# Kernel optimization log

Hardware: AMD Instinct MI355X
Metric: run time of the kernel (lower is better)

## Reference

```python
import math
import jax, jax.numpy as jnp
import numpy as np

S = 2048
HIDDEN = 5120
H = 16              # num_local_heads (128 global heads / TP=8)
NOPE, ROPE, V = 128, 64, 128
QK = NOPE + ROPE    # 192 (module pads to 256; zero-pad is a mathematical no-op)
QLORA, KVLORA = 1536, 512
EPS = 1e-6
BASE, FACTOR = 10000.0, 40.0
BETA_FAST, BETA_SLOW = 32.0, 1.0
ORIG_MAX = 4096
MSCALE = MSCALE_ALL = 0.707


def _yarn_get_mscale(scale, mscale):
    if scale <= 1:
        return 1.0
    return 0.1 * mscale * math.log(scale) + 1.0


SCALING = QK ** -0.5 * _yarn_get_mscale(FACTOR, MSCALE_ALL) ** 2
COS_SIN_MSCALE = _yarn_get_mscale(FACTOR, MSCALE) / _yarn_get_mscale(FACTOR, MSCALE_ALL)


def _yarn_inv_freq():
    half = ROPE // 2
    i = np.arange(half, dtype=np.float64)
    pos_freqs = BASE ** (2.0 * i / ROPE)
    inv_extra = 1.0 / pos_freqs
    inv_interp = 1.0 / (FACTOR * pos_freqs)

    def corr_dim(n_rot):
        return ROPE * math.log(ORIG_MAX / (n_rot * 2 * math.pi)) / (2 * math.log(BASE))

    low = max(math.floor(corr_dim(BETA_FAST)), 0)
    high = min(math.ceil(corr_dim(BETA_SLOW)), ROPE - 1)
    ramp = np.clip((i - low) / max(high - low, 1e-3), 0.0, 1.0)
    inv_freq_mask = 1.0 - ramp  # 1 -> extrapolation, 0 -> interpolation
    inv_freq = inv_interp * (1.0 - inv_freq_mask) + inv_extra * inv_freq_mask
    return jnp.asarray(inv_freq, dtype=jnp.float32)


INV_FREQ = _yarn_inv_freq()  # [ROPE/2]


def _apply_rope(x, cos, sin):
    # non-neox (interleaved pairs): x [S, heads, ROPE], cos/sin [S, ROPE/2]
    x1 = x[..., 0::2]
    x2 = x[..., 1::2]
    c = cos[:, None, :]
    s = sin[:, None, :]
    o1 = x1 * c - x2 * s
    o2 = x2 * c + x1 * s
    return jnp.stack([o1, o2], axis=-1).reshape(x.shape)


def _rms_norm(x, w):
    var = jnp.mean(x.astype(jnp.float32) ** 2, axis=-1, keepdims=True)
    return (x.astype(jnp.float32) * jax.lax.rsqrt(var + EPS)).astype(x.dtype) * w


def setup_inputs() -> dict:
    key = jax.random.key(0)
    ks = jax.random.split(key, 8)
    sd = 0.02
    return {
        'positions': jnp.arange(S, dtype=jnp.int64 if jax.config.jax_enable_x64 else jnp.int32),
        'hidden_states': jax.random.normal(ks[0], (S, HIDDEN), jnp.float32),
        'w_q_a': jax.random.normal(ks[1], (HIDDEN, QLORA), jnp.float32) * sd,
        'q_a_ln_w': jnp.ones((QLORA,), jnp.float32),
        'w_q_b': jax.random.normal(ks[2], (QLORA, H * QK), jnp.float32) * sd,
        'w_kv_a': jax.random.normal(ks[3], (HIDDEN, KVLORA + ROPE), jnp.float32) * sd,
        'kv_a_ln_w': jnp.ones((KVLORA,), jnp.float32),
        'w_kv_b': jax.random.normal(ks[4], (KVLORA, H * (NOPE + V)), jnp.float32) * sd,
        'w_o': jax.random.normal(ks[5], (H * V, HIDDEN), jnp.float32) * sd,
    }


def reference(positions, hidden_states, w_q_a, q_a_ln_w, w_q_b, w_kv_a, kv_a_ln_w, w_kv_b, w_o):
    # Q low-rank path: q_a_proj -> RMSNorm -> q_b_proj
    q = hidden_states @ w_q_a                       # [S, QLORA]
    q = _rms_norm(q, q_a_ln_w)
    q = (q @ w_q_b).reshape(S, H, QK)               # [S, H, 192]
    q_nope, q_pe = q[..., :NOPE], q[..., NOPE:]

    # KV latent path: shared MQA latent + decoupled rope key
    latent = hidden_states @ w_kv_a                 # [S, KVLORA+ROPE]
    kv_a = _rms_norm(latent[:, :KVLORA], kv_a_ln_w)
    k_pe = latent[:, None, KVLORA:]                 # [S, 1, ROPE]
    kv = (kv_a @ w_kv_b).reshape(S, H, NOPE + V)
    k_nope, v = kv[..., :NOPE], kv[..., NOPE:]

    # partial (decoupled) yarn RoPE on the 64-dim rope slice
    freqs = positions.astype(jnp.float32)[:, None] * INV_FREQ[None, :]
    cos = jnp.cos(freqs) * COS_SIN_MSCALE
    sin = jnp.sin(freqs) * COS_SIN_MSCALE
    q_pe = _apply_rope(q_pe, cos, sin)
    k_pe = _apply_rope(k_pe, cos, sin)

    qf = jnp.concatenate([q_nope, q_pe], axis=-1)   # [S, H, 192]
    kf = jnp.concatenate([k_nope, jnp.broadcast_to(k_pe, (S, H, ROPE))], axis=-1)

    # causal paged-attention prefill; zero-padding head dims to 256 is a no-op
    scores = jnp.einsum('qhd,khd->hqk', qf, kf) * SCALING  # [H, S, S]
    causal = jnp.tril(jnp.ones((S, S), dtype=bool))
    scores = jnp.where(causal[None], scores, -jnp.inf)
    probs = jax.nn.softmax(scores, axis=-1)
    attn = jnp.einsum('hqk,khd->qhd', probs, v).reshape(S, H * V)
    return attn @ w_o                               # [S, HIDDEN]
```

## Files before the change

### kernel.cpp

```cpp
#include <hip/hip_runtime.h>
#include <math.h>

typedef unsigned short u16;
typedef unsigned int u32;
typedef __attribute__((ext_vector_type(4))) float f32x4;
typedef __attribute__((ext_vector_type(8))) unsigned short u16x8;
typedef __attribute__((ext_vector_type(4))) unsigned short u16x4;
typedef __attribute__((ext_vector_type(8))) __bf16 bf16x8;

#define DEV __device__ __forceinline__

constexpr int S = 2048;
constexpr int HIDDEN = 5120;
constexpr int H = 16;
constexpr int NOPE = 128, ROPE_D = 64, VD = 128;
constexpr int QKD = NOPE + ROPE_D;
constexpr int QLORA = 1536, KVLORA = 512;
constexpr int KVA_N = KVLORA + ROPE_D;
constexpr float SCALING = 0.11472134f;

DEV u16 f2b(float f) {
  u32 u = __builtin_bit_cast(u32, f);
  u32 r = u + 0x7FFFu + ((u >> 16) & 1u);
  return (u16)(r >> 16);
}
DEV float b2f(u16 h) { return __builtin_bit_cast(float, (u32)h << 16); }

DEV void store_out(float* p, float v) { *p = v; }
DEV void store_out(u16* p, float v) { *p = f2b(v); }

DEV void gload_lds16(const u16* g, u16* l) {
  auto* gp = (const __attribute__((address_space(1))) u16*)g;
  auto* lp = (__attribute__((address_space(3))) u16*)l;
  __builtin_amdgcn_global_load_lds(gp, lp, 16, 0, 0);
}

#define SWZ(row, col) ((col) ^ (((row) & 7) << 3))

__global__ __launch_bounds__(256) void k_convert(const float* __restrict__ in,
                                                 u16* __restrict__ out, int n) {
  int i = (blockIdx.x * 256 + threadIdx.x) * 4;
  if (i >= n) return;
  f32x4 v = *reinterpret_cast<const f32x4*>(in + i);
  u16x4 o;
  o[0] = f2b(v[0]); o[1] = f2b(v[1]); o[2] = f2b(v[2]); o[3] = f2b(v[3]);
  *reinterpret_cast<u16x4*>(out + i) = o;
}

__global__ __launch_bounds__(256) void k_transpose(const float* __restrict__ in,
                                                   u16* __restrict__ out, int R, int C) {
  __shared__ float t[32][33];
  int c0 = blockIdx.x * 32, r0 = blockIdx.y * 32;
  int tx = threadIdx.x, ty = threadIdx.y;
  for (int r = ty; r < 32; r += 8)
    t[r][tx] = in[(size_t)(r0 + r) * C + c0 + tx];
  __syncthreads();
  for (int r = ty; r < 32; r += 8)
    out[(size_t)(c0 + r) * R + r0 + tx] = f2b(t[tx][r]);
}

__global__ __launch_bounds__(256) void k_rope_tables(float* __restrict__ cs,
                                                     float* __restrict__ sn) {
  int idx = blockIdx.x * 256 + threadIdx.x;
  if (idx >= S * 32) return;
  int s = idx >> 5, j = idx & 31;
  double pf = pow(10000.0, (double)j / 32.0);
  double inv_extra = 1.0 / pf;
  double inv_interp = 1.0 / (40.0 * pf);
  double twopi = 6.283185307179586476925286766559;
  double lnb2 = 2.0 * log(10000.0);
  double lowd = floor(64.0 * log(4096.0 / (32.0 * twopi)) / lnb2);
  if (lowd < 0.0) lowd = 0.0;
  double highd = ceil(64.0 * log(4096.0 / twopi) / lnb2);
  if (highd > 63.0) highd = 63.0;
  double denom = highd - lowd;
  if (denom < 0.001) denom = 0.001;
  double ramp = ((double)j - lowd) / denom;
  ramp = ramp < 0.0 ? 0.0 : (ramp > 1.0 ? 1.0 : ramp);
  float invf = (float)(inv_interp * ramp + inv_extra * (1.0 - ramp));
  float fr = (float)s * invf;
  cs[idx] = cosf(fr);
  sn[idx] = sinf(fr);
}

template <typename OutT>
DEV void gemm_body(u16* Al, u16* Bl, const u16* __restrict__ A,
                   const u16* __restrict__ BT, OutT* __restrict__ C,
                   int N, int K, int mbase, int nbase) {
  const int tid = threadIdx.x;
  const int lane = tid & 63, wave = tid >> 6;
  const int wr = wave >> 1, wc = wave & 1;
  const int lr = lane & 15, lk = lane >> 4;
  const int srow = wave * 32 + (lane >> 2);
  const int skoff = (lane & 3) * 8;
  const u16* aptr = A + (size_t)(mbase + srow) * K + skoff;
  const u16* bptr = BT + (size_t)(nbase + srow) * K + skoff;
  u16* alw = Al + wave * (32 * 32);
  u16* blw = Bl + wave * (32 * 32);

  auto STAGE = [&](int b, int kk) {
    gload_lds16(aptr + kk, alw + b * 4096);
    gload_lds16(aptr + (size_t)16 * K + kk, alw + b * 4096 + 16 * 32);
    gload_lds16(bptr + kk, blw + b * 4096);
    gload_lds16(bptr + (size_t)16 * K + kk, blw + b * 4096 + 16 * 32);
  };

  f32x4 acc[4][4];
#pragma unroll
  for (int mf = 0; mf < 4; ++mf)
#pragma unroll
    for (int nf = 0; nf < 4; ++nf) acc[mf][nf] = {0.f, 0.f, 0.f, 0.f};

  const int nt = K >> 5;
  STAGE(0, 0);
  STAGE(1, 32);
  for (int t = 0; t < nt; ++t) {
    const int cur = t & 1;
    if (t + 1 < nt)
      asm volatile("s_waitcnt vmcnt(4)" ::: "memory");
    else
      asm volatile("s_waitcnt vmcnt(0)" ::: "memory");
    __builtin_amdgcn_s_barrier();
    const u16* Ac = Al + cur * 4096;
    const u16* Bc = Bl + cur * 4096;
    bf16x8 af[4], bfr[4];
#pragma unroll
    for (int mf = 0; mf < 4; ++mf)
      af[mf] = *reinterpret_cast<const bf16x8*>(Ac + (wr * 64 + mf * 16 + lr) * 32 + lk * 8);
#pragma unroll
    for (int nf = 0; nf < 4; ++nf)
      bfr[nf] = *reinterpret_cast<const bf16x8*>(Bc + (wc * 64 + nf * 16 + lr) * 32 + lk * 8);
#pragma unroll
    for (int mf = 0; mf < 4; ++mf)
#pragma unroll
      for (int nf = 0; nf < 4; ++nf)
        acc[mf][nf] = __builtin_amdgcn_mfma_f32_16x16x32_bf16(af[mf], bfr[nf], acc[mf][nf], 0, 0, 0);
    __builtin_amdgcn_s_barrier();
    if (t + 2 < nt) STAGE(cur, (t + 2) * 32);
  }

#pragma unroll
  for (int mf = 0; mf < 4; ++mf)
#pragma unroll
    for (int nf = 0; nf < 4; ++nf) {
      int col = nbase + wc * 64 + nf * 16 + lr;
      if (col < N) {
#pragma unroll
        for (int r = 0; r < 4; ++r) {
          int row = mbase + wr * 64 + mf * 16 + lk * 4 + r;
          store_out(&C[(size_t)row * N + col], acc[mf][nf][r]);
        }
      }
    }
}

template <typename OutT>
__global__ __launch_bounds__(256) void k_gemm(const u16* __restrict__ A,
                                              const u16* __restrict__ BT,
                                              OutT* __restrict__ C, int N, int K) {
  __shared__ u16 Al[2 * 128 * 32];
  __shared__ u16 Bl[2 * 128 * 32];
  gemm_body(Al, Bl, A, BT, C, N, K, blockIdx.y * 128, blockIdx.x * 128);
}

template <typename OutT>
__global__ __launch_bounds__(256) void k_gemm2(const u16* __restrict__ A0, const u16* __restrict__ B0,
                                               OutT* __restrict__ C0, int N0, int K0, int nbx0,
                                               const u16* __restrict__ A1, const u16* __restrict__ B1,
                                               OutT* __restrict__ C1, int N1, int K1) {
  __shared__ u16 Al[2 * 128 * 32];
  __shared__ u16 Bl[2 * 128 * 32];
  int bx = blockIdx.x;
  if (bx < nbx0)
    gemm_body(Al, Bl, A0, B0, C0, N0, K0, blockIdx.y * 128, bx * 128);
  else
    gemm_body(Al, Bl, A1, B1, C1, N1, K1, blockIdx.y * 128, (bx - nbx0) * 128);
}

__global__ __launch_bounds__(256) void k_rmsnorm(const float* __restrict__ x,
                                                 const float* __restrict__ w,
                                                 u16* __restrict__ y, int ncols, int instride) {
  int row = blockIdx.x, tid = threadIdx.x;
  const float* xr = x + (size_t)row * instride;
  float ss = 0.f;
  for (int i = tid * 4; i < ncols; i += 1024) {
    f32x4 v = *reinterpret_cast<const f32x4*>(xr + i);
    ss += v[0] * v[0] + v[1] * v[1] + v[2] * v[2] + v[3] * v[3];
  }
  for (int off = 32; off > 0; off >>= 1) ss += __shfl_down(ss, off);
  __shared__ float red[4];
  if ((tid & 63) == 0) red[tid >> 6] = ss;
  __syncthreads();
  ss = red[0] + red[1] + red[2] + red[3];
  float sc = rsqrtf(ss / (float)ncols + 1e-6f);
  u16* yr = y + (size_t)row * ncols;
  for (int i = tid * 4; i < ncols; i += 1024) {
    f32x4 v = *reinterpret_cast<const f32x4*>(xr + i);
    u16x4 o;
    o[0] = f2b(v[0] * sc * w[i]);
    o[1] = f2b(v[1] * sc * w[i + 1]);
    o[2] = f2b(v[2] * sc * w[i + 2]);
    o[3] = f2b(v[3] * sc * w[i + 3]);
    *reinterpret_cast<u16x4*>(yr + i) = o;
  }
}

__global__ __launch_bounds__(256) void k_build_qkf(const u16* __restrict__ qn,
                                                   const u16* __restrict__ kv,
                                                   const float* __restrict__ latent,
                                                   const float* __restrict__ cs,
                                                   const float* __restrict__ sn,
                                                   u16* __restrict__ qf, u16* __restrict__ kf) {
  int s = blockIdx.x, tid = threadIdx.x;
  for (int idx = tid; idx < H * NOPE; idx += 256) {
    int h = idx >> 7, dd = idx & 127;
    qf[((size_t)h * S + s) * QKD + dd] = qn[(size_t)s * (H * QKD) + h * QKD + dd];
    kf[((size_t)h * S + s) * QKD + dd] = kv[(size_t)s * (H * 256) + h * 256 + dd];
  }
  for (int idx = tid; idx < H * 32; idx += 256) {
    int h = idx >> 5, j = idx & 31;
    float c = cs[s * 32 + j], si = sn[s * 32 + j];
    float x1 = b2f(qn[(size_t)s * (H * QKD) + h * QKD + NOPE + 2 * j]);
    float x2 = b2f(qn[(size_t)s * (H * QKD) + h * QKD + NOPE + 2 * j + 1]);
    qf[((size_t)h * S + s) * QKD + NOPE + 2 * j] = f2b(x1 * c - x2 * si);
    qf[((size_t)h * S + s) * QKD + NOPE + 2 * j + 1] = f2b(x2 * c + x1 * si);
    float k1 = latent[(size_t)s * KVA_N + KVLORA + 2 * j];
    float k2 = latent[(size_t)s * KVA_N + KVLORA + 2 * j + 1];
    kf[((size_t)h * S + s) * QKD + NOPE + 2 * j] = f2b(k1 * c - k2 * si);
    kf[((size_t)h * S + s) * QKD + NOPE + 2 * j + 1] = f2b(k2 * c + k1 * si);
  }
}

__global__ void k_build_vt(const u16* __restrict__ kv, u16* __restrict__ vt) {
  __shared__ u16 t[32][33];
  int s0 = blockIdx.x * 32, d0 = blockIdx.y * 32, h = blockIdx.z;
  int tx = threadIdx.x, ty = threadIdx.y;
  for (int r = ty; r < 32; r += 8)
    t[r][tx] = kv[(size_t)(s0 + r) * (H * 256) + h * 256 + NOPE + d0 + tx];
  __syncthreads();
  for (int r = ty; r < 32; r += 8)
    vt[((size_t)h * VD + d0 + r) * S + s0 + tx] = t[tx][r];
}

__global__ __launch_bounds__(256) void k_attn(const u16* __restrict__ qf,
                                              const u16* __restrict__ kf,
                                              const u16* __restrict__ vt,
                                              u16* __restrict__ attn) {
  const int bidx = blockIdx.x;
  const int j = bidx & 31;
  const int h = bidx >> 5;
  const int qt = (h < 8) ? j : 31 - j;
  const int qbase = qt * 64;
  const int tid = threadIdx.x, wave = tid >> 6, lane = tid & 63;
  const int lr = lane & 15, lk = lane >> 4;
  __shared__ u16 Kl[64][192];
  __shared__ u16 Vl[128][64];
  __shared__ u16 Pl[4][16][64];

  int krow_[6], kofs_[6], vrow_[4], vofs_[4];
#pragma unroll
  for (int i = 0; i < 6; ++i) { int c = tid + i * 256; krow_[i] = c / 24; kofs_[i] = (c % 24) * 8; }
#pragma unroll
  for (int i = 0; i < 4; ++i) { int c = tid + i * 256; vrow_[i] = c >> 3; vofs_[i] = (c & 7) * 8; }
  const u16* kfh = kf + (size_t)h * S * QKD;
  const u16* vth = vt + (size_t)h * VD * S;

  bf16x8 qfrag[6];
  const u16* qrow = qf + ((size_t)h * S + qbase + wave * 16 + lr) * QKD;
#pragma unroll
  for (int d = 0; d < 6; ++d)
    qfrag[d] = *reinterpret_cast<const bf16x8*>(qrow + d * 32 + lk * 8);

  u16x8 kreg[6], vreg[4];
#pragma unroll
  for (int i = 0; i < 6; ++i)
    kreg[i] = *reinterpret_cast<const u16x8*>(kfh + (size_t)krow_[i] * QKD + kofs_[i]);
#pragma unroll
  for (int i = 0; i < 4; ++i)
    vreg[i] = *reinterpret_cast<const u16x8*>(vth + (size_t)vrow_[i] * S + vofs_[i]);

  f32x4 o[8];
#pragma unroll
  for (int f = 0; f < 8; ++f) o[f] = {0.f, 0.f, 0.f, 0.f};
  float m_[4] = {-__builtin_inff(), -__builtin_inff(), -__builtin_inff(), -__builtin_inff()};
  float l_[4] = {0.f, 0.f, 0.f, 0.f};

  const int ktiles = qt + 1;
  for (int kt = 0; kt < ktiles; ++kt) {
    const int kbase = kt * 64;
    __builtin_amdgcn_s_barrier();
#pragma unroll
    for (int i = 0; i < 6; ++i)
      *reinterpret_cast<u16x8*>(&Kl[krow_[i]][SWZ(krow_[i], kofs_[i])]) = kreg[i];
#pragma unroll
    for (int i = 0; i < 4; ++i)
      *reinterpret_cast<u16x8*>(&Vl[vrow_[i]][SWZ(vrow_[i], vofs_[i])]) = vreg[i];
    if (kt + 1 < ktiles) {
      const int nb = kbase + 64;
#pragma unroll
      for (int i = 0; i < 6; ++i)
        kreg[i] = *reinterpret_cast<const u16x8*>(kfh + (size_t)(nb + krow_[i]) * QKD + kofs_[i]);
#pragma unroll
      for (int i = 0; i < 4; ++i)
        vreg[i] = *reinterpret_cast<const u16x8*>(vth + (size_t)vrow_[i] * S + nb + vofs_[i]);
    }
    asm volatile("s_waitcnt lgkmcnt(0)" ::: "memory");
    __builtin_amdgcn_s_barrier();

    f32x4 sacc[4];
#pragma unroll
    for (int nf = 0; nf < 4; ++nf) sacc[nf] = {0.f, 0.f, 0.f, 0.f};
    __builtin_amdgcn_s_setprio(1);
#pragma unroll
    for (int nf = 0; nf < 4; ++nf)
#pragma unroll
      for (int dk = 0; dk < 6; ++dk) {
        int krow = nf * 16 + lr;
        bf16x8 b = *reinterpret_cast<const bf16x8*>(&Kl[krow][SWZ(krow, dk * 32 + lk * 8)]);
        sacc[nf] = __builtin_amdgcn_mfma_f32_16x16x32_bf16(qfrag[dk], b, sacc[nf], 0, 0, 0);
      }
    __builtin_amdgcn_s_setprio(0);

    float sv[4][4];
    float rowmax[4] = {-__builtin_inff(), -__builtin_inff(), -__builtin_inff(), -__builtin_inff()};
#pragma unroll
    for (int nf = 0; nf < 4; ++nf) {
      int kcol = kbase + nf * 16 + lr;
#pragma unroll
      for (int r = 0; r < 4; ++r) {
        float v = sacc[nf][r] * SCALING;
        int qrow_g = qbase + wave * 16 + lk * 4 + r;
        if (kcol > qrow_g) v = -__builtin_inff();
        sv[nf][r] = v;
        rowmax[r] = fmaxf(rowmax[r], v);
      }
    }
#pragma unroll
    for (int r = 0; r < 4; ++r) {
#pragma unroll
      for (int off = 1; off < 16; off <<= 1)
        rowmax[r] = fmaxf(rowmax[r], __shfl_xor(rowmax[r], off));
    }
    float alpha[4], rowsum[4] = {0.f, 0.f, 0.f, 0.f};
#pragma unroll
    for (int r = 0; r < 4; ++r) {
      float mn = fmaxf(m_[r], rowmax[r]);
      alpha[r] = __expf(m_[r] - mn);
      m_[r] = mn;
    }
#pragma unroll
    for (int nf = 0; nf < 4; ++nf)
#pragma unroll
      for (int r = 0; r < 4; ++r) {
        float p = __expf(sv[nf][r] - m_[r]);
        sv[nf][r] = p;
        rowsum[r] += p;
      }
#pragma unroll
    for (int r = 0; r < 4; ++r) {
#pragma unroll
      for (int off = 1; off < 16; off <<= 1) rowsum[r] += __shfl_xor(rowsum[r], off);
      l_[r] = l_[r] * alpha[r] + rowsum[r];
    }
#pragma unroll
    for (int nf = 0; nf < 4; ++nf)
#pragma unroll
      for (int r = 0; r < 4; ++r) {
        int prow = lk * 4 + r;
        Pl[wave][prow][SWZ(prow, nf * 16 + lr)] = f2b(sv[nf][r]);
      }
#pragma unroll
    for (int f = 0; f < 8; ++f)
#pragma unroll
      for (int r = 0; r < 4; ++r) o[f][r] *= alpha[r];

    __builtin_amdgcn_s_setprio(1);
#pragma unroll
    for (int kk = 0; kk < 2; ++kk) {
      bf16x8 pa = *reinterpret_cast<const bf16x8*>(&Pl[wave][lr][SWZ(lr, kk * 32 + lk * 8)]);
#pragma unroll
      for (int f = 0; f < 8; ++f) {
        int vrow = f * 16 + lr;
        bf16x8 b = *reinterpret_cast<const bf16x8*>(&Vl[vrow][SWZ(vrow, kk * 32 + lk * 8)]);
        o[f] = __builtin_amdgcn_mfma_f32_16x16x32_bf16(pa, b, o[f], 0, 0, 0);
      }
    }
    __builtin_amdgcn_s_setprio(0);
  }

#pragma unroll
  for (int f = 0; f < 8; ++f)
#pragma unroll
    for (int r = 0; r < 4; ++r) {
      int row = qbase + wave * 16 + lk * 4 + r;
      float val = o[f][r] / l_[r];
      attn[(size_t)row * (H * VD) + h * VD + f * 16 + lr] = f2b(val);
    }
}

extern "C" void kernel_launch(void* const* d_in, const int* in_sizes, int n_in,
                              void* d_out, int out_size, void* d_ws, size_t ws_size,
                              hipStream_t stream) {
  (void)in_sizes; (void)n_in; (void)out_size; (void)ws_size;
  const float* hidden    = (const float*)d_in[1];
  const float* w_q_a     = (const float*)d_in[2];
  const float* q_a_ln_w  = (const float*)d_in[3];
  const float* w_q_b     = (const float*)d_in[4];
  const float* w_kv_a    = (const float*)d_in[5];
  const float* kv_a_ln_w = (const float*)d_in[6];
  const float* w_kv_b    = (const float*)d_in[7];
  const float* w_o       = (const float*)d_in[8];
  float* out = (float*)d_out;

  char* ws = (char*)d_ws;
  size_t off = 0;
  auto alloc = [&](size_t bytes) {
    size_t o = off;
    off += (bytes + 255) & ~(size_t)255;
    return o;
  };
  constexpr int KVA_PAD = 640;
  size_t o_hs    = alloc((size_t)S * HIDDEN * 2);
  size_t o_btqa  = alloc((size_t)QLORA * HIDDEN * 2);
  size_t o_btkva = alloc((size_t)KVA_PAD * HIDDEN * 2);
  size_t o_btqb  = alloc((size_t)(H * QKD) * QLORA * 2);
  size_t o_btkvb = alloc((size_t)(H * 256) * KVLORA * 2);
  size_t o_qlat  = alloc((size_t)S * QLORA * 4);
  size_t o_lat   = alloc((size_t)S * KVA_N * 4);
  size_t o_qln   = alloc((size_t)S * QLORA * 2);
  size_t o_kvln  = alloc((size_t)S * KVLORA * 2);
  size_t o_qn    = alloc((size_t)S * (H * QKD) * 2);
  size_t o_kv    = alloc((size_t)S * (H * 256) * 2);
  size_t o_kf    = alloc((size_t)H * S * QKD * 2);
  size_t o_vt    = alloc((size_t)H * VD * S * 2);
  size_t o_cs    = alloc((size_t)S * 32 * 4);
  size_t o_sn    = alloc((size_t)S * 32 * 4);

  u16* hs_bf  = (u16*)(ws + o_hs);
  u16* bt_qa  = (u16*)(ws + o_btqa);
  u16* bt_kva = (u16*)(ws + o_btkva);
  u16* bt_qb  = (u16*)(ws + o_btqb);
  u16* bt_kvb = (u16*)(ws + o_btkvb);
  float* q_lat  = (float*)(ws + o_qlat);
  float* latent = (float*)(ws + o_lat);
  u16* q_ln  = (u16*)(ws + o_qln);
  u16* kv_ln = (u16*)(ws + o_kvln);
  u16* qn    = (u16*)(ws + o_qn);
  u16* kvb   = (u16*)(ws + o_kv);
  u16* kf    = (u16*)(ws + o_kf);
  u16* vt    = (u16*)(ws + o_vt);
  float* cs = (float*)(ws + o_cs);
  float* sn = (float*)(ws + o_sn);
  u16* qf   = (u16*)(ws + o_hs);
  u16* bt_o = (u16*)(ws + o_btqa);
  u16* attn = (u16*)(ws + o_qlat);

  dim3 t256(256), t32x8(32, 8);

  k_convert<<<(S * HIDDEN / 4 + 255) / 256, t256, 0, stream>>>(hidden, hs_bf, S * HIDDEN);
  k_transpose<<<dim3(QLORA / 32, HIDDEN / 32), t32x8, 0, stream>>>(w_q_a, bt_qa, HIDDEN, QLORA);
  k_transpose<<<dim3(KVA_N / 32, HIDDEN / 32), t32x8, 0, stream>>>(w_kv_a, bt_kva, HIDDEN, KVA_N);
  k_transpose<<<dim3(H * QKD / 32, QLORA / 32), t32x8, 0, stream>>>(w_q_b, bt_qb, QLORA, H * QKD);
  k_transpose<<<dim3(H * 256 / 32, KVLORA / 32), t32x8, 0, stream>>>(w_kv_b, bt_kvb, KVLORA, H * 256);
  k_rope_tables<<<(S * 32 + 255) / 256, t256, 0, stream>>>(cs, sn);

  k_gemm2<float><<<dim3(QLORA / 128 + KVA_PAD / 128, S / 128), t256, 0, stream>>>(
      hs_bf, bt_qa, q_lat, QLORA, HIDDEN, QLORA / 128,
      hs_bf, bt_kva, latent, KVA_N, HIDDEN);

  k_rmsnorm<<<S, t256, 0, stream>>>(q_lat, q_a_ln_w, q_ln, QLORA, QLORA);
  k_rmsnorm<<<S, t256, 0, stream>>>(latent, kv_a_ln_w, kv_ln, KVLORA, KVA_N);

  k_gemm2<u16><<<dim3((H * QKD) / 128 + (H * 256) / 128, S / 128), t256, 0, stream>>>(
      q_ln, bt_qb, qn, H * QKD, QLORA, (H * QKD) / 128,
      kv_ln, bt_kvb, kvb, H * 256, KVLORA);

  k_build_qkf<<<S, t256, 0, stream>>>(qn, kvb, latent, cs, sn, qf, kf);
  k_build_vt<<<dim3(S / 32, VD / 32, H), t32x8, 0, stream>>>(kvb, vt);

  k_transpose<<<dim3(HIDDEN / 32, (H * VD) / 32), t32x8, 0, stream>>>(w_o, bt_o, H * VD, HIDDEN);

  k_attn<<<dim3(512), t256, 0, stream>>>(qf, kf, vt, attn);

  k_gemm<float><<<dim3(HIDDEN / 128, S / 128), t256, 0, stream>>>(attn, bt_o, out, S * 0 + HIDDEN, H * VD);
}
```

Measured before the change: 380.6 us.

## Split-K the first projection GEMM and swizzle GEMM LDS layout

The first down-projection GEMM is split into two K halves, writing separate fp32 partial outputs that are summed inside the RMSNorm and RoPE-building kernels. This doubles the block count so the grid fills the CUs better. Separately, the LDS tile layout of all GEMMs gets an XOR swizzle on the k-chunk index to reduce bank conflicts on fragment reads. The cost is extra partial-buffer memory traffic and workspace.

```diff
diff --git a/kernel.cpp b/kernel.cpp
--- a/kernel.cpp
+++ b/kernel.cpp
@@ -86,23 +86,24 @@
 template <typename OutT>
 DEV void gemm_body(u16* Al, u16* Bl, const u16* __restrict__ A,
                    const u16* __restrict__ BT, OutT* __restrict__ C,
-                   int N, int K, int mbase, int nbase) {
+                   int N, int Kstride, int Klen, int mbase, int nbase) {
   const int tid = threadIdx.x;
   const int lane = tid & 63, wave = tid >> 6;
   const int wr = wave >> 1, wc = wave & 1;
   const int lr = lane & 15, lk = lane >> 4;
   const int srow = wave * 32 + (lane >> 2);
-  const int skoff = (lane & 3) * 8;
-  const u16* aptr = A + (size_t)(mbase + srow) * K + skoff;
-  const u16* bptr = BT + (size_t)(nbase + srow) * K + skoff;
+  const int skoff = (((lane & 3) ^ ((lane >> 3) & 3))) * 8;
+  const int swlk8 = (lk ^ ((lr >> 1) & 3)) * 8;
+  const u16* aptr = A + (size_t)(mbase + srow) * Kstride + skoff;
+  const u16* bptr = BT + (size_t)(nbase + srow) * Kstride + skoff;
   u16* alw = Al + wave * (32 * 32);
   u16* blw = Bl + wave * (32 * 32);
 
   auto STAGE = [&](int b, int kk) {
     gload_lds16(aptr + kk, alw + b * 4096);
-    gload_lds16(aptr + (size_t)16 * K + kk, alw + b * 4096 + 16 * 32);
+    gload_lds16(aptr + (size_t)16 * Kstride + kk, alw + b * 4096 + 16 * 32);
     gload_lds16(bptr + kk, blw + b * 4096);
-    gload_lds16(bptr + (size_t)16 * K + kk, blw + b * 4096 + 16 * 32);
+    gload_lds16(bptr + (size_t)16 * Kstride + kk, blw + b * 4096 + 16 * 32);
   };
 
   f32x4 acc[4][4];
@@ -111,7 +112,7 @@
 #pragma unroll
     for (int nf = 0; nf < 4; ++nf) acc[mf][nf] = {0.f, 0.f, 0.f, 0.f};
 
-  const int nt = K >> 5;
+  const int nt = Klen >> 5;
   STAGE(0, 0);
   STAGE(1, 32);
   for (int t = 0; t < nt; ++t) {
@@ -126,10 +127,10 @@
     bf16x8 af[4], bfr[4];
 #pragma unroll
     for (int mf = 0; mf < 4; ++mf)
-      af[mf] = *reinterpret_cast<const bf16x8*>(Ac + (wr * 64 + mf * 16 + lr) * 32 + lk * 8);
+      af[mf] = *reinterpret_cast<const bf16x8*>(Ac + (wr * 64 + mf * 16 + lr) * 32 + swlk8);
 #pragma unroll
     for (int nf = 0; nf < 4; ++nf)
-      bfr[nf] = *reinterpret_cast<const bf16x8*>(Bc + (wc * 64 + nf * 16 + lr) * 32 + lk * 8);
+      bfr[nf] = *reinterpret_cast<const bf16x8*>(Bc + (wc * 64 + nf * 16 + lr) * 32 + swlk8);
 #pragma unroll
     for (int mf = 0; mf < 4; ++mf)
 #pragma unroll
@@ -160,7 +161,7 @@
                                               OutT* __restrict__ C, int N, int K) {
   __shared__ u16 Al[2 * 128 * 32];
   __shared__ u16 Bl[2 * 128 * 32];
-  gemm_body(Al, Bl, A, BT, C, N, K, blockIdx.y * 128, blockIdx.x * 128);
+  gemm_body(Al, Bl, A, BT, C, N, K, K, blockIdx.y * 128, blockIdx.x * 128);
 }
 
 template <typename OutT>
@@ -172,19 +173,44 @@
   __shared__ u16 Bl[2 * 128 * 32];
   int bx = blockIdx.x;
   if (bx < nbx0)
-    gemm_body(Al, Bl, A0, B0, C0, N0, K0, blockIdx.y * 128, bx * 128);
+    gemm_body(Al, Bl, A0, B0, C0, N0, K0, K0, blockIdx.y * 128, bx * 128);
   else
-    gemm_body(Al, Bl, A1, B1, C1, N1, K1, blockIdx.y * 128, (bx - nbx0) * 128);
-}
-
-__global__ __launch_bounds__(256) void k_rmsnorm(const float* __restrict__ x,
-                                                 const float* __restrict__ w,
-                                                 u16* __restrict__ y, int ncols, int instride) {
+    gemm_body(Al, Bl, A1, B1, C1, N1, K1, K1, blockIdx.y * 128, (bx - nbx0) * 128);
+}
+
+__global__ __launch_bounds__(256) void k_gemm_dp(const u16* __restrict__ A,
+                                                 const u16* __restrict__ Bq,
+                                                 const u16* __restrict__ Bkv,
+                                                 float* __restrict__ q0, float* __restrict__ q1,
+                                                 float* __restrict__ l0, float* __restrict__ l1) {
+  __shared__ u16 Al[2 * 128 * 32];
+  __shared__ u16 Bl[2 * 128 * 32];
+  constexpr int KH = HIDDEN / 2;
+  int bx = blockIdx.x;
+  int split = bx >= 17;
+  int j = bx - split * 17;
+  const u16* As = A + split * KH;
+  if (j < 12) {
+    gemm_body(Al, Bl, As, Bq + split * KH, split ? q1 : q0, QLORA, HIDDEN, KH,
+              blockIdx.y * 128, j * 128);
+  } else {
+    gemm_body(Al, Bl, As, Bkv + split * KH, split ? l1 : l0, KVA_N, HIDDEN, KH,
+              blockIdx.y * 128, (j - 12) * 128);
+  }
+}
+
+__global__ __launch_bounds__(256) void k_rmsnorm2(const float* __restrict__ x0,
+                                                  const float* __restrict__ x1,
+                                                  const float* __restrict__ w,
+                                                  u16* __restrict__ y, int ncols, int instride) {
   int row = blockIdx.x, tid = threadIdx.x;
-  const float* xr = x + (size_t)row * instride;
+  const float* xr0 = x0 + (size_t)row * instride;
+  const float* xr1 = x1 + (size_t)row * instride;
   float ss = 0.f;
   for (int i = tid * 4; i < ncols; i += 1024) {
-    f32x4 v = *reinterpret_cast<const f32x4*>(xr + i);
+    f32x4 a = *reinterpret_cast<const f32x4*>(xr0 + i);
+    f32x4 b = *reinterpret_cast<const f32x4*>(xr1 + i);
+    f32x4 v = a + b;
     ss += v[0] * v[0] + v[1] * v[1] + v[2] * v[2] + v[3] * v[3];
   }
   for (int off = 32; off > 0; off >>= 1) ss += __shfl_down(ss, off);
@@ -195,7 +221,9 @@
   float sc = rsqrtf(ss / (float)ncols + 1e-6f);
   u16* yr = y + (size_t)row * ncols;
   for (int i = tid * 4; i < ncols; i += 1024) {
-    f32x4 v = *reinterpret_cast<const f32x4*>(xr + i);
+    f32x4 a = *reinterpret_cast<const f32x4*>(xr0 + i);
+    f32x4 b = *reinterpret_cast<const f32x4*>(xr1 + i);
+    f32x4 v = a + b;
     u16x4 o;
     o[0] = f2b(v[0] * sc * w[i]);
     o[1] = f2b(v[1] * sc * w[i + 1]);
@@ -207,7 +235,8 @@
 
 __global__ __launch_bounds__(256) void k_build_qkf(const u16* __restrict__ qn,
                                                    const u16* __restrict__ kv,
-                                                   const float* __restrict__ latent,
+                                                   const float* __restrict__ lat0,
+                                                   const float* __restrict__ lat1,
                                                    const float* __restrict__ cs,
                                                    const float* __restrict__ sn,
                                                    u16* __restrict__ qf, u16* __restrict__ kf) {
@@ -224,8 +253,8 @@
     float x2 = b2f(qn[(size_t)s * (H * QKD) + h * QKD + NOPE + 2 * j + 1]);
     qf[((size_t)h * S + s) * QKD + NOPE + 2 * j] = f2b(x1 * c - x2 * si);
     qf[((size_t)h * S + s) * QKD + NOPE + 2 * j + 1] = f2b(x2 * c + x1 * si);
-    float k1 = latent[(size_t)s * KVA_N + KVLORA + 2 * j];
-    float k2 = latent[(size_t)s * KVA_N + KVLORA + 2 * j + 1];
+    float k1 = lat0[(size_t)s * KVA_N + KVLORA + 2 * j] + lat1[(size_t)s * KVA_N + KVLORA + 2 * j];
+    float k2 = lat0[(size_t)s * KVA_N + KVLORA + 2 * j + 1] + lat1[(size_t)s * KVA_N + KVLORA + 2 * j + 1];
     kf[((size_t)h * S + s) * QKD + NOPE + 2 * j] = f2b(k1 * c - k2 * si);
     kf[((size_t)h * S + s) * QKD + NOPE + 2 * j + 1] = f2b(k2 * c + k1 * si);
   }
@@ -425,8 +454,10 @@
   size_t o_btkva = alloc((size_t)KVA_PAD * HIDDEN * 2);
   size_t o_btqb  = alloc((size_t)(H * QKD) * QLORA * 2);
   size_t o_btkvb = alloc((size_t)(H * 256) * KVLORA * 2);
-  size_t o_qlat  = alloc((size_t)S * QLORA * 4);
-  size_t o_lat   = alloc((size_t)S * KVA_N * 4);
+  size_t o_qlat0 = alloc((size_t)S * QLORA * 4);
+  size_t o_qlat1 = alloc((size_t)S * QLORA * 4);
+  size_t o_lat0  = alloc((size_t)S * KVA_N * 4);
+  size_t o_lat1  = alloc((size_t)S * KVA_N * 4);
   size_t o_qln   = alloc((size_t)S * QLORA * 2);
   size_t o_kvln  = alloc((size_t)S * KVLORA * 2);
   size_t o_qn    = alloc((size_t)S * (H * QKD) * 2);
@@ -441,8 +472,10 @@
   u16* bt_kva = (u16*)(ws + o_btkva);
   u16* bt_qb  = (u16*)(ws + o_btqb);
   u16* bt_kvb = (u16*)(ws + o_btkvb);
-  float* q_lat  = (float*)(ws + o_qlat);
-  float* latent = (float*)(ws + o_lat);
+  float* q_lat0 = (float*)(ws + o_qlat0);
+  float* q_lat1 = (float*)(ws + o_qlat1);
+  float* lat0   = (float*)(ws + o_lat0);
+  float* lat1   = (float*)(ws + o_lat1);
   u16* q_ln  = (u16*)(ws + o_qln);
   u16* kv_ln = (u16*)(ws + o_kvln);
   u16* qn    = (u16*)(ws + o_qn);
@@ -453,7 +486,7 @@
   float* sn = (float*)(ws + o_sn);
   u16* qf   = (u16*)(ws + o_hs);
   u16* bt_o = (u16*)(ws + o_btqa);
-  u16* attn = (u16*)(ws + o_qlat);
+  u16* attn = (u16*)(ws + o_qlat0);
 
   dim3 t256(256), t32x8(32, 8);
 
@@ -464,23 +497,22 @@
   k_transpose<<<dim3(H * 256 / 32, KVLORA / 32), t32x8, 0, stream>>>(w_kv_b, bt_kvb, KVLORA, H * 256);
   k_rope_tables<<<(S * 32 + 255) / 256, t256, 0, stream>>>(cs, sn);
 
-  k_gemm2<float><<<dim3(QLORA / 128 + KVA_PAD / 128, S / 128), t256, 0, stream>>>(
-      hs_bf, bt_qa, q_lat, QLORA, HIDDEN, QLORA / 128,
-      hs_bf, bt_kva, latent, KVA_N, HIDDEN);
-
-  k_rmsnorm<<<S, t256, 0, stream>>>(q_lat, q_a_ln_w, q_ln, QLORA, QLORA);
-  k_rmsnorm<<<S, t256, 0, stream>>>(latent, kv_a_ln_w, kv_ln, KVLORA, KVA_N);
+  k_gemm_dp<<<dim3(34, S / 128), t256, 0, stream>>>(hs_bf, bt_qa, bt_kva,
+                                                    q_lat0, q_lat1, lat0, lat1);
+
+  k_rmsnorm2<<<S, t256, 0, stream>>>(q_lat0, q_lat1, q_a_ln_w, q_ln, QLORA, QLORA);
+  k_rmsnorm2<<<S, t256, 0, stream>>>(lat0, lat1, kv_a_ln_w, kv_ln, KVLORA, KVA_N);
 
   k_gemm2<u16><<<dim3((H * QKD) / 128 + (H * 256) / 128, S / 128), t256, 0, stream>>>(
       q_ln, bt_qb, qn, H * QKD, QLORA, (H * QKD) / 128,
       kv_ln, bt_kvb, kvb, H * 256, KVLORA);
 
-  k_build_qkf<<<S, t256, 0, stream>>>(qn, kvb, latent, cs, sn, qf, kf);
+  k_build_qkf<<<S, t256, 0, stream>>>(qn, kvb, lat0, lat1, cs, sn, qf, kf);
   k_build_vt<<<dim3(S / 32, VD / 32, H), t32x8, 0, stream>>>(kvb, vt);
 
   k_transpose<<<dim3(HIDDEN / 32, (H * VD) / 32), t32x8, 0, stream>>>(w_o, bt_o, H * VD, HIDDEN);
 
   k_attn<<<dim3(512), t256, 0, stream>>>(qf, kf, vt, attn);
 
-  k_gemm<float><<<dim3(HIDDEN / 128, S / 128), t256, 0, stream>>>(attn, bt_o, out, S * 0 + HIDDEN, H * VD);
-}
+  k_gemm<float><<<dim3(HIDDEN / 128, S / 128), t256, 0, stream>>>(attn, bt_o, out, HIDDEN, H * VD);
+}
```

New measurement: 378.3 us. No clear change (-0.6%).

## Enlarge GEMM tiles to 256-wide with 4-stage pipeline, LDS swizzle, 8 waves

Applied to the files above, without the earlier changes.

Rewrites the shared GEMM body to use 512-thread blocks with 128x256 or 256x256 tiles and a 4-deep global-to-LDS prefetch ring. It also XOR-swizzles the LDS layout to avoid bank conflicts and raises wave priority around the MFMA loop. The projection GEMMs get dedicated kernels with flattened grids sized to the new tiles, and the kv_a weight padding grows to 768 to fit 256-wide column tiles. The aim is more data reuse per tile and better latency hiding, at the cost of more LDS per block and fewer blocks, which may leave CUs idle on the smaller GEMMs.

```diff
diff --git a/kernel.cpp b/kernel.cpp
--- a/kernel.cpp
+++ b/kernel.cpp
@@ -83,98 +83,133 @@
   sn[idx] = sinf(fr);
 }
 
-template <typename OutT>
+template <int BM, typename OutT>
 DEV void gemm_body(u16* Al, u16* Bl, const u16* __restrict__ A,
                    const u16* __restrict__ BT, OutT* __restrict__ C,
                    int N, int K, int mbase, int nbase) {
+  constexpr int MF = BM / 32;
+  constexpr int ABUF = BM * 32;
+  constexpr int BBUF = 256 * 32;
+  constexpr int L = (BM == 256) ? 4 : 3;
   const int tid = threadIdx.x;
   const int lane = tid & 63, wave = tid >> 6;
-  const int wr = wave >> 1, wc = wave & 1;
+  const int wm = wave >> 2, wn = wave & 3;
   const int lr = lane & 15, lk = lane >> 4;
-  const int srow = wave * 32 + (lane >> 2);
-  const int skoff = (lane & 3) * 8;
-  const u16* aptr = A + (size_t)(mbase + srow) * K + skoff;
-  const u16* bptr = BT + (size_t)(nbase + srow) * K + skoff;
-  u16* alw = Al + wave * (32 * 32);
-  u16* blw = Bl + wave * (32 * 32);
+  const int srowB = wave * 32 + (lane >> 2);
+  const int srowA = (BM == 256) ? srowB : (wave * 16 + (lane >> 2));
+  const int skoff = ((lane & 3) ^ ((lane >> 3) & 3)) * 8;
+  const int swlk8 = (lk ^ ((lr >> 1) & 3)) * 8;
+  const u16* aptr = A + (size_t)(mbase + srowA) * K + skoff;
+  const u16* bptr = BT + (size_t)(nbase + srowB) * K + skoff;
+  u16* alw = Al + wave * ((BM == 256) ? 1024 : 512);
+  u16* blw = Bl + wave * 1024;
 
   auto STAGE = [&](int b, int kk) {
-    gload_lds16(aptr + kk, alw + b * 4096);
-    gload_lds16(aptr + (size_t)16 * K + kk, alw + b * 4096 + 16 * 32);
-    gload_lds16(bptr + kk, blw + b * 4096);
-    gload_lds16(bptr + (size_t)16 * K + kk, blw + b * 4096 + 16 * 32);
+    gload_lds16(aptr + kk, alw + b * ABUF);
+    if constexpr (BM == 256) gload_lds16(aptr + (size_t)16 * K + kk, alw + b * ABUF + 512);
+    gload_lds16(bptr + kk, blw + b * BBUF);
+    gload_lds16(bptr + (size_t)16 * K + kk, blw + b * BBUF + 512);
   };
 
-  f32x4 acc[4][4];
-#pragma unroll
-  for (int mf = 0; mf < 4; ++mf)
+  f32x4 acc[MF][4];
+#pragma unroll
+  for (int mf = 0; mf < MF; ++mf)
 #pragma unroll
     for (int nf = 0; nf < 4; ++nf) acc[mf][nf] = {0.f, 0.f, 0.f, 0.f};
 
   const int nt = K >> 5;
   STAGE(0, 0);
   STAGE(1, 32);
+  STAGE(2, 64);
+  STAGE(3, 96);
   for (int t = 0; t < nt; ++t) {
-    const int cur = t & 1;
-    if (t + 1 < nt)
-      asm volatile("s_waitcnt vmcnt(4)" ::: "memory");
-    else
-      asm volatile("s_waitcnt vmcnt(0)" ::: "memory");
+    const int cur = t & 3;
+    const int rem = nt - 1 - t;
+    if constexpr (L == 4) {
+      if (rem >= 3)      asm volatile("s_waitcnt vmcnt(12)" ::: "memory");
+      else if (rem == 2) asm volatile("s_waitcnt vmcnt(8)" ::: "memory");
+      else if (rem == 1) asm volatile("s_waitcnt vmcnt(4)" ::: "memory");
+      else               asm volatile("s_waitcnt vmcnt(0)" ::: "memory");
+    } else {
+      if (rem >= 3)      asm volatile("s_waitcnt vmcnt(9)" ::: "memory");
+      else if (rem == 2) asm volatile("s_waitcnt vmcnt(6)" ::: "memory");
+      else if (rem == 1) asm volatile("s_waitcnt vmcnt(3)" ::: "memory");
+      else               asm volatile("s_waitcnt vmcnt(0)" ::: "memory");
+    }
     __builtin_amdgcn_s_barrier();
-    const u16* Ac = Al + cur * 4096;
-    const u16* Bc = Bl + cur * 4096;
-    bf16x8 af[4], bfr[4];
-#pragma unroll
-    for (int mf = 0; mf < 4; ++mf)
-      af[mf] = *reinterpret_cast<const bf16x8*>(Ac + (wr * 64 + mf * 16 + lr) * 32 + lk * 8);
-#pragma unroll
-    for (int nf = 0; nf < 4; ++nf)
-      bfr[nf] = *reinterpret_cast<const bf16x8*>(Bc + (wc * 64 + nf * 16 + lr) * 32 + lk * 8);
-#pragma unroll
-    for (int mf = 0; mf < 4; ++mf)
-#pragma unroll
-      for (int nf = 0; nf < 4; ++nf)
-        acc[mf][nf] = __builtin_amdgcn_mfma_f32_16x16x32_bf16(af[mf], bfr[nf], acc[mf][nf], 0, 0, 0);
+    const u16* Ac = Al + cur * ABUF + (wm * (BM / 2)) * 32;
+    const u16* Bc = Bl + cur * BBUF + (wn * 64) * 32;
+    bf16x8 af[MF];
+#pragma unroll
+    for (int mf = 0; mf < MF; ++mf)
+      af[mf] = *reinterpret_cast<const bf16x8*>(Ac + (mf * 16 + lr) * 32 + swlk8);
+    __builtin_amdgcn_s_setprio(1);
+#pragma unroll
+    for (int nf = 0; nf < 4; ++nf) {
+      bf16x8 bfr = *reinterpret_cast<const bf16x8*>(Bc + (nf * 16 + lr) * 32 + swlk8);
+#pragma unroll
+      for (int mf = 0; mf < MF; ++mf)
+        acc[mf][nf] = __builtin_amdgcn_mfma_f32_16x16x32_bf16(af[mf], bfr, acc[mf][nf], 0, 0, 0);
+    }
+    __builtin_amdgcn_s_setprio(0);
     __builtin_amdgcn_s_barrier();
-    if (t + 2 < nt) STAGE(cur, (t + 2) * 32);
-  }
-
-#pragma unroll
-  for (int mf = 0; mf < 4; ++mf)
+    if (t + 4 < nt) STAGE(cur, (t + 4) * 32);
+  }
+
+#pragma unroll
+  for (int mf = 0; mf < MF; ++mf)
 #pragma unroll
     for (int nf = 0; nf < 4; ++nf) {
-      int col = nbase + wc * 64 + nf * 16 + lr;
+      int col = nbase + wn * 64 + nf * 16 + lr;
       if (col < N) {
 #pragma unroll
         for (int r = 0; r < 4; ++r) {
-          int row = mbase + wr * 64 + mf * 16 + lk * 4 + r;
+          int row = mbase + wm * (BM / 2) + mf * 16 + lk * 4 + r;
           store_out(&C[(size_t)row * N + col], acc[mf][nf][r]);
         }
       }
     }
 }
 
-template <typename OutT>
-__global__ __launch_bounds__(256) void k_gemm(const u16* __restrict__ A,
-                                              const u16* __restrict__ BT,
-                                              OutT* __restrict__ C, int N, int K) {
-  __shared__ u16 Al[2 * 128 * 32];
-  __shared__ u16 Bl[2 * 128 * 32];
-  gemm_body(Al, Bl, A, BT, C, N, K, blockIdx.y * 128, blockIdx.x * 128);
-}
-
-template <typename OutT>
-__global__ __launch_bounds__(256) void k_gemm2(const u16* __restrict__ A0, const u16* __restrict__ B0,
-                                               OutT* __restrict__ C0, int N0, int K0, int nbx0,
-                                               const u16* __restrict__ A1, const u16* __restrict__ B1,
-                                               OutT* __restrict__ C1, int N1, int K1) {
-  __shared__ u16 Al[2 * 128 * 32];
-  __shared__ u16 Bl[2 * 128 * 32];
+__global__ __launch_bounds__(512) void k_gemm_dp(const u16* __restrict__ A,
+                                                 const u16* __restrict__ Bq,
+                                                 const u16* __restrict__ Bkv,
+                                                 float* __restrict__ q_lat,
+                                                 float* __restrict__ latent) {
+  __shared__ u16 Al[4 * 128 * 32];
+  __shared__ u16 Bl[4 * 256 * 32];
+  int bid = blockIdx.x;
+  int row = bid & 15, ct = bid >> 4;
+  if (ct < 6)
+    gemm_body<128>(Al, Bl, A, Bq, q_lat, QLORA, HIDDEN, row * 128, ct * 256);
+  else
+    gemm_body<128>(Al, Bl, A, Bkv, latent, KVA_N, HIDDEN, row * 128, (ct - 6) * 256);
+}
+
+__global__ __launch_bounds__(512) void k_gemm_up(const u16* __restrict__ Aq,
+                                                 const u16* __restrict__ Bq,
+                                                 u16* __restrict__ Cq,
+                                                 const u16* __restrict__ Akv,
+                                                 const u16* __restrict__ Bkv,
+                                                 u16* __restrict__ Ckv) {
+  __shared__ u16 Al[4 * 256 * 32];
+  __shared__ u16 Bl[4 * 256 * 32];
   int bx = blockIdx.x;
-  if (bx < nbx0)
-    gemm_body(Al, Bl, A0, B0, C0, N0, K0, blockIdx.y * 128, bx * 128);
-  else
-    gemm_body(Al, Bl, A1, B1, C1, N1, K1, blockIdx.y * 128, (bx - nbx0) * 128);
+  if (bx < 96)
+    gemm_body<256>(Al, Bl, Aq, Bq, Cq, H * QKD, QLORA, (bx & 7) * 256, (bx >> 3) * 256);
+  else {
+    int l = bx - 96;
+    gemm_body<256>(Al, Bl, Akv, Bkv, Ckv, H * 256, KVLORA, (l & 7) * 256, (l >> 3) * 256);
+  }
+}
+
+__global__ __launch_bounds__(512) void k_gemm_out(const u16* __restrict__ A,
+                                                  const u16* __restrict__ BT,
+                                                  float* __restrict__ C) {
+  __shared__ u16 Al[4 * 256 * 32];
+  __shared__ u16 Bl[4 * 256 * 32];
+  int bid = blockIdx.x;
+  gemm_body<256>(Al, Bl, A, BT, C, HIDDEN, H * VD, (bid & 7) * 256, (bid >> 3) * 256);
 }
 
 __global__ __launch_bounds__(256) void k_rmsnorm(const float* __restrict__ x,
@@ -419,7 +454,7 @@
     off += (bytes + 255) & ~(size_t)255;
     return o;
   };
-  constexpr int KVA_PAD = 640;
+  constexpr int KVA_PAD = 768;
   size_t o_hs    = alloc((size_t)S * HIDDEN * 2);
   size_t o_btqa  = alloc((size_t)QLORA * HIDDEN * 2);
   size_t o_btkva = alloc((size_t)KVA_PAD * HIDDEN * 2);
@@ -464,16 +499,12 @@
   k_transpose<<<dim3(H * 256 / 32, KVLORA / 32), t32x8, 0, stream>>>(w_kv_b, bt_kvb, KVLORA, H * 256);
   k_rope_tables<<<(S * 32 + 255) / 256, t256, 0, stream>>>(cs, sn);
 
-  k_gemm2<float><<<dim3(QLORA / 128 + KVA_PAD / 128, S / 128), t256, 0, stream>>>(
-      hs_bf, bt_qa, q_lat, QLORA, HIDDEN, QLORA / 128,
-      hs_bf, bt_kva, latent, KVA_N, HIDDEN);
+  k_gemm_dp<<<dim3(144), dim3(512), 0, stream>>>(hs_bf, bt_qa, bt_kva, q_lat, latent);
 
   k_rmsnorm<<<S, t256, 0, stream>>>(q_lat, q_a_ln_w, q_ln, QLORA, QLORA);
   k_rmsnorm<<<S, t256, 0, stream>>>(latent, kv_a_ln_w, kv_ln, KVLORA, KVA_N);
 
-  k_gemm2<u16><<<dim3((H * QKD) / 128 + (H * 256) / 128, S / 128), t256, 0, stream>>>(
-      q_ln, bt_qb, qn, H * QKD, QLORA, (H * QKD) / 128,
-      kv_ln, bt_kvb, kvb, H * 256, KVLORA);
+  k_gemm_up<<<dim3(224), dim3(512), 0, stream>>>(q_ln, bt_qb, qn, kv_ln, bt_kvb, kvb);
 
   k_build_qkf<<<S, t256, 0, stream>>>(qn, kvb, latent, cs, sn, qf, kf);
   k_build_vt<<<dim3(S / 32, VD / 32, H), t32x8, 0, stream>>>(kvb, vt);
@@ -482,5 +513,5 @@
 
   k_attn<<<dim3(512), t256, 0, stream>>>(qf, kf, vt, attn);
 
-  k_gemm<float><<<dim3(HIDDEN / 128, S / 128), t256, 0, stream>>>(attn, bt_o, out, S * 0 + HIDDEN, H * VD);
-}
+  k_gemm_out<<<dim3(160), dim3(512), 0, stream>>>(attn, bt_o, out);
+}
```

After: 433.9 us. 14.0% more time.
